# Optimization experiments

Measured on AMD Instinct MI355X. Metric: run time of the kernel, lower is better.

The kernel has to match this reference:

```python
import jax, jax.numpy as jnp
import numpy as np

HIDDEN = 256
DEPTH = 4
ATOM_FDIM = 35
BOND_FDIM = 5
MAX_NB = 10
N_ATOMS = 50000
N_BONDS = 100000
N_MESS = 10000
N_PAIRS = 10000
PAIR_K = 2
N_MOLS = 2000
ATOMS_PER_MOL = 25  # N_MOLS * ATOMS_PER_MOL == N_ATOMS


def setup_inputs() -> dict:
    key = jax.random.key(0)
    ks = jax.random.split(key, 10)
    fatoms = jax.random.normal(ks[0], (N_ATOMS, ATOM_FDIM), jnp.float32)
    fbonds = jax.random.normal(ks[1], (N_BONDS, ATOM_FDIM + BOND_FDIM), jnp.float32)
    tree_message = jax.random.normal(ks[2], (N_MESS, HIDDEN), jnp.float32)
    tree_message = tree_message.at[0].set(0.0)  # index 0 is the zero padding message
    agraph = jax.random.randint(ks[3], (N_ATOMS, MAX_NB), 0, N_MESS + N_BONDS)
    bgraph = jax.random.randint(ks[4], (N_BONDS, MAX_NB), 0, N_MESS + N_BONDS)
    pair_idx = jax.random.randint(ks[5], (N_PAIRS, PAIR_K), 0, N_BONDS)
    si = 1.0 / np.sqrt(ATOM_FDIM + BOND_FDIM).astype(np.float32)
    sh = 1.0 / np.sqrt(HIDDEN).astype(np.float32)
    so = 1.0 / np.sqrt(ATOM_FDIM + HIDDEN).astype(np.float32)
    W_i = jax.random.uniform(ks[6], (HIDDEN, ATOM_FDIM + BOND_FDIM), jnp.float32, -si, si)
    W_h = jax.random.uniform(ks[7], (HIDDEN, HIDDEN), jnp.float32, -sh, sh)
    W_o = jax.random.uniform(ks[8], (HIDDEN, ATOM_FDIM + HIDDEN), jnp.float32, -so, so)
    b_o = jax.random.uniform(ks[9], (HIDDEN,), jnp.float32, -so, so)
    return {"fatoms": fatoms, "fbonds": fbonds, "tree_message": tree_message,
            "agraph": agraph, "bgraph": bgraph, "pair_idx": pair_idx,
            "W_i": W_i, "W_h": W_h, "W_o": W_o, "b_o": b_o}


def reference(fatoms, fbonds, tree_message, agraph, bgraph, pair_idx, W_i, W_h, W_o, b_o):
    # binput = W_i(fbonds); graph_message = relu(binput)
    binput = fbonds @ W_i.T                      # [N_BONDS, H]
    graph_message = jax.nn.relu(binput)
    for _ in range(DEPTH - 1):
        message = jnp.concatenate([tree_message, graph_message], axis=0)  # [N_MESS+N_BONDS, H]
        nei_message = message[bgraph].sum(axis=1)  # gather [N_BONDS, MAX_NB, H] -> sum
        graph_message = jax.nn.relu(binput + nei_message @ W_h.T)
    # dict-indexed mean over bonds between tree nodes -> regular [N_PAIRS, K] gather-mean
    collated = graph_message[pair_idx].mean(axis=1)  # [N_PAIRS, H]
    message = jnp.concatenate([tree_message, graph_message], axis=0)
    nei_message = message[agraph].sum(axis=1)        # [N_ATOMS, H]
    ainput = jnp.concatenate([fatoms, nei_message], axis=1)  # [N_ATOMS, 35+H]
    atom_hiddens = jax.nn.relu(ainput @ W_o.T + b_o)
    # scope-based mean pooling (uniform molecules)
    mol_vecs = atom_hiddens.reshape(N_MOLS, ATOMS_PER_MOL, HIDDEN).mean(axis=1)
    return (mol_vecs, collated)
```

## Files before the change

### kernel.cpp

```cpp
#include <hip/hip_runtime.h>


#define H     256
#define NBND  100000
#define NATM  50000
#define NMESS 10000
#define MAXNB 10
#define AF    35
#define BF    40
#define NPAIR 10000
#define NMOL  2000
#define APM   25

typedef unsigned short u16;
typedef unsigned int   u32;
using short8 = __attribute__((ext_vector_type(8))) short;
using f32x4  = __attribute__((ext_vector_type(4))) float;

__device__ __forceinline__ float bflo(u32 w) { return __uint_as_float(w << 16); }
__device__ __forceinline__ float bfhi(u32 w) { return __uint_as_float(w & 0xffff0000u); }
__device__ __forceinline__ u16 f2bf(float f) {
    u32 x = __float_as_uint(f);
    return (u16)((x + 0x7fffu + ((x >> 16) & 1u)) >> 16);
}
__device__ __forceinline__ u32 pack2(float a, float b) {
    return (u32)f2bf(a) | ((u32)f2bf(b) << 16);
}

__global__ __launch_bounds__(256) void k_treecvt(const float* __restrict__ tree_in,
                                                 u16* __restrict__ tree) {
    const long i = ((long)blockIdx.x * 256 + threadIdx.x) * 4;
    float4 v = *(const float4*)(tree_in + i);
    uint2 o;
    o.x = pack2(v.x, v.y);
    o.y = pack2(v.z, v.w);
    *(uint2*)(tree + i) = o;
}

__global__ __launch_bounds__(64) void k_wfrag(const float* __restrict__ Wm, int ldm, int offm,
                                              const float* __restrict__ We, int lde, int nce,
                                              u16* __restrict__ dst) {
    const int t = threadIdx.x;
    const int ks = blockIdx.x >> 4, nt = blockIdx.x & 15;
    const int n = nt * 16 + (t & 15);
    u16 vals[8];
#pragma unroll
    for (int e = 0; e < 8; ++e) {
        const int k = ks * 32 + (t >> 4) * 8 + e;
        float v;
        if (k < 256)            v = Wm[(long)n * ldm + offm + k];
        else if (k - 256 < nce) v = We[(long)n * lde + (k - 256)];
        else                    v = 0.f;
        vals[e] = f2bf(v);
    }
    *(uint4*)(dst + ((size_t)blockIdx.x * 64 + t) * 8) = *(const uint4*)vals;
}

template <int MODE>
__global__ __launch_bounds__(256, 3) void k_main(
        const int* __restrict__ graph, const u16* __restrict__ tree,
        const u16* __restrict__ gm_in, const float* __restrict__ ext,
        const u16* __restrict__ wfrag, const float* __restrict__ b_o,
        u16* __restrict__ out_bf, float* __restrict__ out_f) {
    constexpr int NR  = (MODE == 2) ? NATM : NBND;
    constexpr int EXT = (MODE == 2) ? AF : BF;
    __shared__ __align__(16) u16 a1[64 * 256];
    __shared__ __align__(16) u16 a2[64 * 64];
    __shared__ int idx_lds[64 * MAXNB];

    const int t = threadIdx.x;
    const int lane = t & 63;
    const int w = t >> 6;
    const int r0 = blockIdx.x * 64;

    if (MODE != 0) {
        for (int i = t; i < 64 * MAXNB; i += 256) {
            const int r = r0 + i / MAXNB;
            idx_lds[i] = (r < NR) ? graph[(long)r * MAXNB + i % MAXNB] : 0;
        }
    }
    for (int i = t; i < 64 * 64; i += 256) {
        const int row = i >> 6, k = i & 63;
        const int r = r0 + row;
        const float v = (r < NR && k < EXT) ? ext[(long)r * EXT + k] : 0.f;
        const int bo = (row * 128 + k * 2) ^ ((row & 7) << 4);
        *(u16*)((char*)a2 + bo) = f2bf(v);
    }
    __syncthreads();

    if (MODE != 0) {
        for (int bb = 0; bb < 16; ++bb) {
            const int b = w * 16 + bb;
            float s0 = 0.f, s1 = 0.f, s2 = 0.f, s3 = 0.f;
            if (r0 + b < NR) {
#pragma unroll
                for (int j = 0; j < MAXNB; ++j) {
                    const int idx = __builtin_amdgcn_readfirstlane(idx_lds[b * MAXNB + j]);
                    const u16* p = (idx < NMESS) ? tree + (size_t)idx * H
                                                 : gm_in + (size_t)(idx - NMESS) * H;
                    const uint2 q = *(const uint2*)(p + lane * 4);
                    s0 += bflo(q.x); s1 += bfhi(q.x);
                    s2 += bflo(q.y); s3 += bfhi(q.y);
                }
            }
            uint2 o;
            o.x = pack2(s0, s1);
            o.y = pack2(s2, s3);
            const int bo = (b * 512 + lane * 8) ^ ((b & 7) << 4);
            *(uint2*)((char*)a1 + bo) = o;
        }
        __syncthreads();
    }

    f32x4 acc[4][4];
#pragma unroll
    for (int mt = 0; mt < 4; ++mt)
#pragma unroll
        for (int nt = 0; nt < 4; ++nt) acc[mt][nt] = (f32x4){0.f, 0.f, 0.f, 0.f};

    const short8* wf = (const short8*)wfrag;
    constexpr int KS0 = (MODE == 0) ? 8 : 0;
#pragma unroll
    for (int ks = KS0; ks < 10; ++ks) {
        short8 a[4], bf[4];
#pragma unroll
        for (int mt = 0; mt < 4; ++mt) {
            const int row = mt * 16 + (lane & 15);
            int bo;
            const char* base;
            if (ks < 8) { bo = (row * 512 + (ks * 32 + (lane >> 4) * 8) * 2); base = (const char*)a1; }
            else        { bo = (row * 128 + ((ks - 8) * 32 + (lane >> 4) * 8) * 2); base = (const char*)a2; }
            bo ^= (row & 7) << 4;
            a[mt] = *(const short8*)(base + bo);
        }
#pragma unroll
        for (int nt = 0; nt < 4; ++nt)
            bf[nt] = wf[((size_t)(ks * 16 + (w * 4 + nt)) * 64) + lane];
#pragma unroll
        for (int mt = 0; mt < 4; ++mt)
#pragma unroll
            for (int nt = 0; nt < 4; ++nt)
                acc[mt][nt] = __builtin_amdgcn_mfma_f32_16x16x32_bf16(a[mt], bf[nt], acc[mt][nt], 0, 0, 0);
    }

    float bo4[4];
    if (MODE == 2) {
#pragma unroll
        for (int nt = 0; nt < 4; ++nt) bo4[nt] = b_o[w * 64 + nt * 16 + (lane & 15)];
    }
#pragma unroll
    for (int mt = 0; mt < 4; ++mt) {
#pragma unroll
        for (int nt = 0; nt < 4; ++nt) {
            const int col = w * 64 + nt * 16 + (lane & 15);
#pragma unroll
            for (int r = 0; r < 4; ++r) {
                const int row = r0 + mt * 16 + (lane >> 4) * 4 + r;
                if (row < NR) {
                    const float v = acc[mt][nt][r];
                    if (MODE == 2)
                        out_f[(size_t)row * H + col] = fmaxf(v + bo4[nt], 0.f);
                    else
                        out_bf[(size_t)row * H + col] = f2bf(fmaxf(v, 0.f));
                }
            }
        }
    }
}

__global__ __launch_bounds__(256) void k_collated(const int* __restrict__ pair_idx,
                                                  const u16* __restrict__ gm,
                                                  float* __restrict__ out) {
    const int w = threadIdx.x >> 6, lane = threadIdx.x & 63;
    const long p = (long)blockIdx.x * 4 + w;
    if (p >= NPAIR) return;
    const size_t i0 = (size_t)pair_idx[p * 2 + 0];
    const size_t i1 = (size_t)pair_idx[p * 2 + 1];
    uint2 qa = *(const uint2*)(gm + i0 * H + lane * 4);
    uint2 qb = *(const uint2*)(gm + i1 * H + lane * 4);
    float4 o;
    o.x = 0.5f * (bflo(qa.x) + bflo(qb.x));
    o.y = 0.5f * (bfhi(qa.x) + bfhi(qb.x));
    o.z = 0.5f * (bflo(qa.y) + bflo(qb.y));
    o.w = 0.5f * (bfhi(qa.y) + bfhi(qb.y));
    *(float4*)(out + p * H + lane * 4) = o;
}

__global__ __launch_bounds__(256) void k_molmean(const float* __restrict__ hidden,
                                                 float* __restrict__ out) {
    const int m = blockIdx.x, c = threadIdx.x;
    float s = 0.f;
#pragma unroll
    for (int a = 0; a < APM; ++a)
        s += hidden[((long)m * APM + a) * H + c];
    out[(long)m * H + c] = s * (1.f / APM);
}

extern "C" void kernel_launch(void* const* d_in, const int* in_sizes, int n_in,
                              void* d_out, int out_size, void* d_ws, size_t ws_size,
                              hipStream_t stream) {
    (void)in_sizes; (void)n_in; (void)out_size;
    const float* fatoms  = (const float*)d_in[0];
    const float* fbonds  = (const float*)d_in[1];
    const float* tree_in = (const float*)d_in[2];
    const int* agraph    = (const int*)d_in[3];
    const int* bgraph    = (const int*)d_in[4];
    const int* pair_idx  = (const int*)d_in[5];
    const float* W_i = (const float*)d_in[6];
    const float* W_h = (const float*)d_in[7];
    const float* W_o = (const float*)d_in[8];
    const float* b_o = (const float*)d_in[9];

    float* out = (float*)d_out;

    const size_t WFRAG = 10 * 16 * 64 * 8;
    const size_t need = ((size_t)NMESS + 2 * (size_t)NBND) * H * sizeof(u16)
                        + 2 * WFRAG * sizeof(u16);
    if (ws_size < need) return;

    u16* tree    = (u16*)d_ws;
    u16* gmA     = tree + (size_t)NMESS * H;
    u16* gmB     = gmA + (size_t)NBND * H;
    u16* wfrag_h = gmB + (size_t)NBND * H;
    u16* wfrag_o = wfrag_h + WFRAG;
    float* hidden = (float*)gmA;

    const int GB = (NBND + 63) / 64;
    const int GA = (NATM + 63) / 64;

    k_treecvt<<<(NMESS * H) / 1024, 256, 0, stream>>>(tree_in, tree);
    k_wfrag<<<160, 64, 0, stream>>>(W_h, 256, 0, W_i, BF, BF, wfrag_h);
    k_wfrag<<<160, 64, 0, stream>>>(W_o, 291, AF, W_o, 291, AF, wfrag_o);

    k_main<0><<<GB, 256, 0, stream>>>(nullptr, tree, gmA, fbonds, wfrag_h, nullptr, gmA, nullptr);
    k_main<1><<<GB, 256, 0, stream>>>(bgraph, tree, gmA, fbonds, wfrag_h, nullptr, gmB, nullptr);
    k_main<1><<<GB, 256, 0, stream>>>(bgraph, tree, gmB, fbonds, wfrag_h, nullptr, gmA, nullptr);
    k_main<1><<<GB, 256, 0, stream>>>(bgraph, tree, gmA, fbonds, wfrag_h, nullptr, gmB, nullptr);
    k_collated<<<NPAIR / 4, 256, 0, stream>>>(pair_idx, gmB, out + (size_t)NMOL * H);
    k_main<2><<<GA, 256, 0, stream>>>(agraph, tree, gmB, fatoms, wfrag_o, b_o, nullptr, hidden);
    k_molmean<<<NMOL, 256, 0, stream>>>(hidden, out);
}
```

Baseline: 437.2 us.

## Load external features directly into MFMA fragments and raise occupancy

Removes the a2 shared-memory staging buffer for the atom/bond feature columns. The MFMA A-fragments for the last two k-steps are now built directly from global fp32 loads converted to bf16 in registers, which drops one LDS buffer and one barrier. Launch bounds go from 3 to 4 blocks per CU, and the neighbor indices for each row are read into registers before the gather loop so the loads can be issued together. In exchange, global feature loads become less coalesced, with scalar loads for the 35-wide atom rows, and the row-validity check on the gather is dropped.

```diff
diff --git a/kernel.cpp b/kernel.cpp
--- a/kernel.cpp
+++ b/kernel.cpp
@@ -57,15 +57,37 @@
 }
 
 template <int MODE>
-__global__ __launch_bounds__(256, 3) void k_main(
+__device__ __forceinline__ short8 ldext_frag(const float* __restrict__ ext,
+                                             int rr, int lane, int ks, int NR) {
+    constexpr int EXT = (MODE == 2) ? AF : BF;
+    const int c0 = (ks == 9 ? 32 : 0) + ((lane >> 4) * 8);
+    union { short8 s; u32 u[4]; u16 h[8]; } cv;
+    cv.u[0] = cv.u[1] = cv.u[2] = cv.u[3] = 0;
+    if (rr >= NR || c0 >= EXT) return cv.s;
+    const float* p = ext + (size_t)rr * EXT + c0;
+    if (MODE != 2) {
+        float4 v0 = *(const float4*)p;
+        float4 v1 = *(const float4*)(p + 4);
+        cv.u[0] = pack2(v0.x, v0.y);
+        cv.u[1] = pack2(v0.z, v0.w);
+        cv.u[2] = pack2(v1.x, v1.y);
+        cv.u[3] = pack2(v1.z, v1.w);
+    } else {
+#pragma unroll
+        for (int e = 0; e < 8; ++e)
+            cv.h[e] = (c0 + e < EXT) ? f2bf(p[e]) : (u16)0;
+    }
+    return cv.s;
+}
+
+template <int MODE>
+__global__ __launch_bounds__(256, 4) void k_main(
         const int* __restrict__ graph, const u16* __restrict__ tree,
         const u16* __restrict__ gm_in, const float* __restrict__ ext,
         const u16* __restrict__ wfrag, const float* __restrict__ b_o,
         u16* __restrict__ out_bf, float* __restrict__ out_f) {
-    constexpr int NR  = (MODE == 2) ? NATM : NBND;
-    constexpr int EXT = (MODE == 2) ? AF : BF;
+    constexpr int NR = (MODE == 2) ? NATM : NBND;
     __shared__ __align__(16) u16 a1[64 * 256];
-    __shared__ __align__(16) u16 a2[64 * 64];
     __shared__ int idx_lds[64 * MAXNB];
 
     const int t = threadIdx.x;
@@ -78,30 +100,21 @@
             const int r = r0 + i / MAXNB;
             idx_lds[i] = (r < NR) ? graph[(long)r * MAXNB + i % MAXNB] : 0;
         }
-    }
-    for (int i = t; i < 64 * 64; i += 256) {
-        const int row = i >> 6, k = i & 63;
-        const int r = r0 + row;
-        const float v = (r < NR && k < EXT) ? ext[(long)r * EXT + k] : 0.f;
-        const int bo = (row * 128 + k * 2) ^ ((row & 7) << 4);
-        *(u16*)((char*)a2 + bo) = f2bf(v);
-    }
-    __syncthreads();
-
-    if (MODE != 0) {
+        __syncthreads();
         for (int bb = 0; bb < 16; ++bb) {
             const int b = w * 16 + bb;
+            int id[MAXNB];
+#pragma unroll
+            for (int j = 0; j < MAXNB; ++j)
+                id[j] = __builtin_amdgcn_readfirstlane(idx_lds[b * MAXNB + j]);
             float s0 = 0.f, s1 = 0.f, s2 = 0.f, s3 = 0.f;
-            if (r0 + b < NR) {
-#pragma unroll
-                for (int j = 0; j < MAXNB; ++j) {
-                    const int idx = __builtin_amdgcn_readfirstlane(idx_lds[b * MAXNB + j]);
-                    const u16* p = (idx < NMESS) ? tree + (size_t)idx * H
-                                                 : gm_in + (size_t)(idx - NMESS) * H;
-                    const uint2 q = *(const uint2*)(p + lane * 4);
-                    s0 += bflo(q.x); s1 += bfhi(q.x);
-                    s2 += bflo(q.y); s3 += bfhi(q.y);
-                }
+#pragma unroll
+            for (int j = 0; j < MAXNB; ++j) {
+                const u16* p = (id[j] < NMESS) ? tree + (size_t)id[j] * H
+                                               : gm_in + (size_t)(id[j] - NMESS) * H;
+                const uint2 q = *(const uint2*)(p + lane * 4);
+                s0 += bflo(q.x); s1 += bfhi(q.x);
+                s2 += bflo(q.y); s3 += bfhi(q.y);
             }
             uint2 o;
             o.x = pack2(s0, s1);
@@ -126,12 +139,12 @@
 #pragma unroll
         for (int mt = 0; mt < 4; ++mt) {
             const int row = mt * 16 + (lane & 15);
-            int bo;
-            const char* base;
-            if (ks < 8) { bo = (row * 512 + (ks * 32 + (lane >> 4) * 8) * 2); base = (const char*)a1; }
-            else        { bo = (row * 128 + ((ks - 8) * 32 + (lane >> 4) * 8) * 2); base = (const char*)a2; }
-            bo ^= (row & 7) << 4;
-            a[mt] = *(const short8*)(base + bo);
+            if (ks < 8) {
+                const int bo = (row * 512 + (ks * 32 + (lane >> 4) * 8) * 2) ^ ((row & 7) << 4);
+                a[mt] = *(const short8*)((const char*)a1 + bo);
+            } else {
+                a[mt] = ldext_frag<MODE>(ext, r0 + row, lane, ks, NR);
+            }
         }
 #pragma unroll
         for (int nt = 0; nt < 4; ++nt)
```

Result: faster. 371.8 us (-15.0%).
